# Performance work log

Measured on AMD Instinct MI355X. Metric: run time of the kernel, lower is better.

## Reference

```python
import jax, jax.numpy as jnp
import numpy as np

N = 30000
E = 480000
C_IN, H = 16, 4
NEG_SLOPE = 0.2  # PyG GATv2Conv default negative_slope


def gatv2(x, src, dst, Wl, bl, Wr, br, att, bias, heads, outc, concat, n):
    # PyG GATv2Conv (share_weights=False): e_ij = att . leaky_relu(Wl x_j + Wr x_i)
    xl = (x @ Wl + bl).reshape(n, heads, outc)   # source transform
    xr = (x @ Wr + br).reshape(n, heads, outc)   # target transform
    e = jax.nn.leaky_relu(xl[src] + xr[dst], NEG_SLOPE)        # [E,H,C]
    logits = jnp.einsum('ehc,hc->eh', e, att)                  # [E,H]
    m = jax.lax.stop_gradient(jax.ops.segment_max(logits, dst, num_segments=n))
    ex = jnp.exp(logits - m[dst])
    denom = jax.ops.segment_sum(ex, dst, num_segments=n)
    alpha = ex / denom[dst]                                    # scatter-softmax over in-edges
    out = jax.ops.segment_sum(alpha[:, :, None] * xl[src], dst, num_segments=n)  # [N,H,C]
    out = out.reshape(n, heads * outc) if concat else out.mean(axis=1)
    return out + bias


def setup_inputs() -> dict:
    key = jax.random.key(0)
    ks = jax.random.split(key, 16)
    s = 0.05
    inp = {
        'x': jax.random.uniform(ks[0], (N, C_IN), dtype=jnp.float32),
        'edge_index': jax.random.randint(ks[1], (2, E), 0, N, dtype=jnp.int32),
        'lower_bound': jnp.zeros((C_IN,), jnp.float32),
        'upper_bound': jnp.ones((C_IN,), jnp.float32),
        # Layer 1: GATv2Conv(16 -> 32 per head, heads=4, concat=True) => 128
        'W1l': jax.random.normal(ks[2], (C_IN, H * 32), jnp.float32) * s,
        'b1l': jnp.zeros((H * 32,), jnp.float32),
        'W1r': jax.random.normal(ks[3], (C_IN, H * 32), jnp.float32) * s,
        'b1r': jnp.zeros((H * 32,), jnp.float32),
        'att1': jax.random.normal(ks[4], (H, 32), jnp.float32) * s,
        'bias1': jnp.zeros((H * 32,), jnp.float32),
        # Layer 2: GATv2Conv(128 -> 64 per head, heads=4, concat=False) => 64
        'W2l': jax.random.normal(ks[5], (128, H * 64), jnp.float32) * s,
        'b2l': jnp.zeros((H * 64,), jnp.float32),
        'W2r': jax.random.normal(ks[6], (128, H * 64), jnp.float32) * s,
        'b2r': jnp.zeros((H * 64,), jnp.float32),
        'att2': jax.random.normal(ks[7], (H, 64), jnp.float32) * s,
        'bias2': jnp.zeros((64,), jnp.float32),
        # Final linear head 64 -> 5
        'W3': jax.random.normal(ks[8], (64, 5), jnp.float32) * s,
        'b3': jnp.zeros((5,), jnp.float32),
    }
    return inp


def reference(x, edge_index, lower_bound, upper_bound,
              W1l, b1l, W1r, b1r, att1, bias1,
              W2l, b2l, W2r, b2r, att2, bias2,
              W3, b3):
    n = x.shape[0]
    # min-max normalization
    y = (x - lower_bound) / (upper_bound - lower_bound)
    # add self loops (PyG GATv2Conv default add_self_loops=True)
    loops = jnp.tile(jnp.arange(n, dtype=edge_index.dtype)[None, :], (2, 1))
    ei = jnp.concatenate([edge_index, loops], axis=1)
    src, dst = ei[0], ei[1]
    y = gatv2(y, src, dst, W1l, b1l, W1r, b1r, att1, bias1, H, 32, True, n)
    y = jax.nn.relu(y)
    y = gatv2(y, src, dst, W2l, b2l, W2r, b2r, att2, bias2, H, 64, False, n)
    y = jax.nn.relu(y)
    y = y @ W3 + b3
    return jax.nn.sigmoid(y)
```

## Files before the change

kernel.cpp:

```cpp
#include <hip/hip_runtime.h>

#define H 4
#define D1 128
#define D2 256
#define CIN 16
#define SLOPE 0.2f
#define LOG2E 1.4426950408889634f

typedef short short8v __attribute__((ext_vector_type(8)));
typedef float float4v __attribute__((ext_vector_type(4)));
typedef float float2v __attribute__((ext_vector_type(2)));

__device__ __forceinline__ float bflo(unsigned u) { return __uint_as_float(u << 16); }
__device__ __forceinline__ float bfdirty(unsigned u) { return __uint_as_float(u); }
__device__ __forceinline__ unsigned short f2bf(float f) {
    unsigned int u = __float_as_uint(f);
    u += 0x7FFFu + ((u >> 16) & 1u);
    return (unsigned short)(u >> 16);
}
__device__ __forceinline__ unsigned short f2fp8x2(float a, float b) {
    return (unsigned short)__builtin_amdgcn_cvt_pk_fp8_f32(a, b, 0, false);
}

__global__ void k_hist(const int* __restrict__ ei, int E, int ET,
                       int* __restrict__ deg) {
    int idx = blockIdx.x * blockDim.x + threadIdx.x;
    if (idx >= ET) return;
    int dst = (idx < E) ? ei[E + idx] : idx - E;
    atomicAdd(&deg[dst], 1);
}

__global__ __launch_bounds__(1024) void k_scan_one(
        const int* __restrict__ deg, int* __restrict__ rp,
        int* __restrict__ cur, int n) {
    __shared__ int wsum[16];
    int t = threadIdx.x;
    int lane = t & 63, w = t >> 6;
    int base = t * 32;
    int vals[32];
    const int4* dp = (const int4*)deg;
#pragma unroll
    for (int q = 0; q < 8; ++q) {
        int4 v = dp[(base >> 2) + q];
        vals[4 * q + 0] = v.x; vals[4 * q + 1] = v.y;
        vals[4 * q + 2] = v.z; vals[4 * q + 3] = v.w;
    }
    int loc[32];
    int s = 0;
#pragma unroll
    for (int k = 0; k < 32; ++k) {
        int idx = base + k;
        int v = (idx < n) ? vals[k] : 0;
        loc[k] = s;
        s += v;
    }
    int inc = s;
#pragma unroll
    for (int off = 1; off < 64; off <<= 1) {
        int u = __shfl_up(inc, off, 64);
        if (lane >= off) inc += u;
    }
    int excl = inc - s;
    if (lane == 63) wsum[w] = inc;
    __syncthreads();
    if (w == 0) {
        int v = (lane < 16) ? wsum[lane] : 0;
        int winc = v;
#pragma unroll
        for (int off = 1; off < 16; off <<= 1) {
            int u = __shfl_up(winc, off, 64);
            if (lane >= off) winc += u;
        }
        if (lane < 16) wsum[lane] = winc - v;
    }
    __syncthreads();
    int offw = wsum[w] + excl;
#pragma unroll
    for (int q = 0; q < 8; ++q) {
        int i0 = base + 4 * q;
        if (i0 + 3 < n) {
            *(int4*)(rp + i0) = make_int4(offw + loc[4 * q + 0], offw + loc[4 * q + 1],
                                          offw + loc[4 * q + 2], offw + loc[4 * q + 3]);
            *(int4*)(cur + i0) = make_int4(0, 0, 0, 0);
        } else {
#pragma unroll
            for (int e = 0; e < 4; ++e) {
                int idx = i0 + e;
                if (idx < n) { rp[idx] = offw + loc[4 * q + e]; cur[idx] = 0; }
            }
        }
    }
}

__global__ void k_fill(const int* __restrict__ ei, int E, int ET,
                       const int* __restrict__ rp, int* __restrict__ cur,
                       int* __restrict__ eord) {
    int idx = blockIdx.x * blockDim.x + threadIdx.x;
    if (idx >= ET) return;
    int src, dst;
    if (idx < E) { src = ei[idx]; dst = ei[E + idx]; }
    else         { src = dst = idx - E; }
    int pos = atomicAdd(&cur[dst], 1);
    eord[rp[dst] + pos] = src;
}

__global__ __launch_bounds__(256) void k_prep(
        const float* __restrict__ x, const float* __restrict__ lb,
        const float* __restrict__ ub,
        const float* __restrict__ Wl, const float* __restrict__ bl,
        const float* __restrict__ Wr, const float* __restrict__ br,
        unsigned char* __restrict__ xl8, float* __restrict__ xr,
        const float* __restrict__ W2l, const float* __restrict__ W2r,
        unsigned short* __restrict__ W2t,
        int* __restrict__ deg, int n, int B1) {
    __shared__ float Wls[CIN][D1];
    __shared__ float Wrs[CIN][D1];
    __shared__ float ys[16][CIN];
    int b = blockIdx.x;
    int t = threadIdx.x;
    if (b >= B1) {
        int rb = b - B1;
        if (rb < 256) {
            int idx = rb * 256 + t;
            int k = idx >> 9, c = idx & 511;
            float v = (c < 256) ? W2l[k * 256 + c] : W2r[k * 256 + (c - 256)];
            W2t[(size_t)c * 128 + k] = f2bf(v);
        } else {
            int idx = (rb - 256) * 256 + t;
            if (idx < n) deg[idx] = 0;
        }
        return;
    }
    int i0 = b * 16;
#pragma unroll
    for (int i = 0; i < 8; ++i) {
        int flat = t + 256 * i;
        int k = flat >> 7, c = flat & 127;
        Wls[k][c] = Wl[k * D1 + c];
        Wrs[k][c] = Wr[k * D1 + c];
    }
    {
        int node = t >> 4, k = t & 15;
        int gi = i0 + node;
        float xv = (gi < n) ? x[(size_t)gi * CIN + k] : 0.f;
        ys[node][k] = (xv - lb[k]) / (ub[k] - lb[k]);
    }
    __syncthreads();
    int c = t & 127;
    bool left = t < 128;
    const float (*Ws)[D1] = left ? Wls : Wrs;
    float bias = left ? bl[c] : br[c];
    for (int j = 0; j < 16; ++j) {
        float acc = bias;
#pragma unroll
        for (int k = 0; k < CIN; ++k) acc += ys[j][k] * Ws[k][c];
        int gi = i0 + j;
        float other = __shfl_xor(acc, 1);
        if (gi < n) {
            if (left) {
                if (!(c & 1))
                    *(unsigned short*)(xl8 + (size_t)gi * D1 + c) = f2fp8x2(acc, other);
            } else {
                xr[(size_t)gi * D1 + c] = acc;
            }
        }
    }
}

__global__ __launch_bounds__(256) void k_lin2_mfma(
        const unsigned short* __restrict__ h1b,
        const unsigned short* __restrict__ W2t,
        const float* __restrict__ b2l, const float* __restrict__ b2r,
        unsigned char* __restrict__ xl2,
        unsigned short* __restrict__ xr2,
        int n) {
    __shared__ unsigned short At[128 * 128];
    __shared__ unsigned short Bt[128 * 128];
    int t = threadIdx.x;
    int row0 = blockIdx.x * 128;
    int col0 = blockIdx.y * 128;

    {
        int r = t >> 1, hh = (t & 1) * 64;
        bool ok = (row0 + r) < n;
        const unsigned short* gA = h1b + (size_t)(row0 + r) * 128 + hh;
        const unsigned short* gB = W2t + (size_t)(col0 + r) * 128 + hh;
#pragma unroll
        for (int i = 0; i < 8; ++i) {
            uint4 vA = ok ? *(const uint4*)(gA + i * 8) : make_uint4(0, 0, 0, 0);
            uint4 vB = *(const uint4*)(gB + i * 8);
            int col = hh + i * 8;
            int idx = (r * 128 + col) ^ ((r & 15) << 3);
            *(uint4*)&At[idx] = vA;
            *(uint4*)&Bt[idx] = vB;
        }
    }
    __syncthreads();

    int w = t >> 6, l = t & 63;
    int wr = w >> 1, wc = w & 1;
    float4v acc[4][4];
#pragma unroll
    for (int m = 0; m < 4; ++m)
#pragma unroll
        for (int nn = 0; nn < 4; ++nn) acc[m][nn] = (float4v)0.f;

#pragma unroll
    for (int ks = 0; ks < 4; ++ks) {
        int kb = ks * 32 + ((l >> 4) << 3);
        short8v a[4], b[4];
#pragma unroll
        for (int m = 0; m < 4; ++m) {
            int r = wr * 64 + m * 16 + (l & 15);
            a[m] = *(const short8v*)&At[(r * 128 + kb) ^ ((r & 15) << 3)];
        }
#pragma unroll
        for (int nn = 0; nn < 4; ++nn) {
            int c = wc * 64 + nn * 16 + (l & 15);
            b[nn] = *(const short8v*)&Bt[(c * 128 + kb) ^ ((c & 15) << 3)];
        }
#pragma unroll
        for (int m = 0; m < 4; ++m)
#pragma unroll
            for (int nn = 0; nn < 4; ++nn)
                acc[m][nn] = __builtin_amdgcn_mfma_f32_16x16x32_bf16(
                    a[m], b[nn], acc[m][nn], 0, 0, 0);
    }

    if (col0 < 256) {
        const float* bp = b2l;
        int cb = col0;
#pragma unroll
        for (int nn = 0; nn < 4; ++nn) {
            int colc = cb + wc * 64 + nn * 16 + (l & 15);
            float bv = bp[colc];
#pragma unroll
            for (int m = 0; m < 4; ++m) {
                int rbase = row0 + wr * 64 + m * 16 + ((l >> 4) << 2);
#pragma unroll
                for (int r = 0; r < 4; ++r) {
                    int row = rbase + r;
                    float val = acc[m][nn][r] + bv;
                    float other = __shfl_xor(val, 1);
                    if (!(l & 1) && row < n)
                        *(unsigned short*)(xl2 + (size_t)row * 256 + colc) =
                            f2fp8x2(val, other);
                }
            }
        }
    } else {
        const float* bp = b2r;
        int cb = col0 - 256;
#pragma unroll
        for (int nn = 0; nn < 4; ++nn) {
            int colc = cb + wc * 64 + nn * 16 + (l & 15);
            float bv = bp[colc];
#pragma unroll
            for (int m = 0; m < 4; ++m) {
                int rbase = row0 + wr * 64 + m * 16 + ((l >> 4) << 2);
#pragma unroll
                for (int r = 0; r < 4; ++r) {
                    int row = rbase + r;
                    if (row < n)
                        xr2[(size_t)row * 256 + colc] = f2bf(acc[m][nn][r] + bv);
                }
            }
        }
    }
}

__global__ __launch_bounds__(256) void k_agg1(
        const unsigned char* __restrict__ xl8, const float* __restrict__ xr,
        const float* __restrict__ att, const float* __restrict__ bias,
        const int* __restrict__ rp, const int* __restrict__ deg,
        const int* __restrict__ eord, unsigned short* __restrict__ h1b, int n) {
    int t = threadIdx.x;
    int node = blockIdx.x * 4 + (t >> 6);
    int l = t & 63;
    int nd = (node < n) ? node : n - 1;
    float2 xrv = *(const float2*)(xr + (size_t)nd * D1 + 2 * l);
    float2 av  = *(const float2*)(att + 2 * l);
    av.x *= LOG2E; av.y *= LOG2E;
    int start = __builtin_amdgcn_readfirstlane(rp[nd]);
    int cnt   = (node < n) ? deg[nd] : 0;
    cnt = __builtin_amdgcn_readfirstlane(cnt);
    const unsigned short* xlp = (const unsigned short*)xl8;
    float d = 0.f, a0 = 0.f, a1 = 0.f;
    int cnt4 = cnt & ~3;
    unsigned r0, r1, r2, r3;
    if (cnt4 > 0) {
        int i0 = eord[start + 0], i1 = eord[start + 1];
        int i2 = eord[start + 2], i3 = eord[start + 3];
        r0 = xlp[(size_t)i0 * 64 + l]; r1 = xlp[(size_t)i1 * 64 + l];
        r2 = xlp[(size_t)i2 * 64 + l]; r3 = xlp[(size_t)i3 * 64 + l];
    }
    for (int j = 0; j < cnt4; j += 4) {
        unsigned p0 = r0, p1 = r1, p2 = r2, p3 = r3;
        int jn = j + 4;
        if (jn < cnt4) {
            int i0 = eord[start + jn + 0], i1 = eord[start + jn + 1];
            int i2 = eord[start + jn + 2], i3 = eord[start + jn + 3];
            r0 = xlp[(size_t)i0 * 64 + l]; r1 = xlp[(size_t)i1 * 64 + l];
            r2 = xlp[(size_t)i2 * 64 + l]; r3 = xlp[(size_t)i3 * 64 + l];
        }
        float2v f0 = __builtin_amdgcn_cvt_pk_f32_fp8(p0, false);
        float2v f1 = __builtin_amdgcn_cvt_pk_f32_fp8(p1, false);
        float2v f2 = __builtin_amdgcn_cvt_pk_f32_fp8(p2, false);
        float2v f3 = __builtin_amdgcn_cvt_pk_f32_fp8(p3, false);
        float x00 = f0.x, x01 = f0.y;
        float x10 = f1.x, x11 = f1.y;
        float x20 = f2.x, x21 = f2.y;
        float x30 = f3.x, x31 = f3.y;
        float v, lg0, lg1, lg2, lg3;
        v = x00 + xrv.x; v = fmaxf(v, SLOPE * v); lg0  = av.x * v;
        v = x01 + xrv.y; v = fmaxf(v, SLOPE * v); lg0 += av.y * v;
        v = x10 + xrv.x; v = fmaxf(v, SLOPE * v); lg1  = av.x * v;
        v = x11 + xrv.y; v = fmaxf(v, SLOPE * v); lg1 += av.y * v;
        v = x20 + xrv.x; v = fmaxf(v, SLOPE * v); lg2  = av.x * v;
        v = x21 + xrv.y; v = fmaxf(v, SLOPE * v); lg2 += av.y * v;
        v = x30 + xrv.x; v = fmaxf(v, SLOPE * v); lg3  = av.x * v;
        v = x31 + xrv.y; v = fmaxf(v, SLOPE * v); lg3 += av.y * v;
        lg0 += __shfl_xor(lg0, 8); lg1 += __shfl_xor(lg1, 8);
        lg2 += __shfl_xor(lg2, 8); lg3 += __shfl_xor(lg3, 8);
        lg0 += __shfl_xor(lg0, 4); lg1 += __shfl_xor(lg1, 4);
        lg2 += __shfl_xor(lg2, 4); lg3 += __shfl_xor(lg3, 4);
        lg0 += __shfl_xor(lg0, 2); lg1 += __shfl_xor(lg1, 2);
        lg2 += __shfl_xor(lg2, 2); lg3 += __shfl_xor(lg3, 2);
        lg0 += __shfl_xor(lg0, 1); lg1 += __shfl_xor(lg1, 1);
        lg2 += __shfl_xor(lg2, 1); lg3 += __shfl_xor(lg3, 1);
        float e0 = exp2f(lg0), e1 = exp2f(lg1);
        float e2 = exp2f(lg2), e3 = exp2f(lg3);
        d += (e0 + e1) + (e2 + e3);
        a0 += e0 * x00 + e1 * x10 + e2 * x20 + e3 * x30;
        a1 += e0 * x01 + e1 * x11 + e2 * x21 + e3 * x31;
    }
    for (int j = cnt4; j < cnt; ++j) {
        int s0 = eord[start + j];
        unsigned p0 = xlp[(size_t)s0 * 64 + l];
        float2v f0 = __builtin_amdgcn_cvt_pk_f32_fp8(p0, false);
        float x00 = f0.x, x01 = f0.y;
        float v, lg0;
        v = x00 + xrv.x; v = fmaxf(v, SLOPE * v); lg0  = av.x * v;
        v = x01 + xrv.y; v = fmaxf(v, SLOPE * v); lg0 += av.y * v;
        lg0 += __shfl_xor(lg0, 8);
        lg0 += __shfl_xor(lg0, 4);
        lg0 += __shfl_xor(lg0, 2);
        lg0 += __shfl_xor(lg0, 1);
        float e0 = exp2f(lg0);
        d += e0;
        a0 += e0 * x00;
        a1 += e0 * x01;
    }
    if (node < n) {
        float inv = 1.f / d;
        float o0 = fmaxf(a0 * inv + bias[2 * l + 0], 0.f);
        float o1 = fmaxf(a1 * inv + bias[2 * l + 1], 0.f);
        ((unsigned*)h1b)[(size_t)node * 64 + l] =
            ((unsigned)f2bf(o1) << 16) | f2bf(o0);
    }
}

__global__ __launch_bounds__(256) void k_agg2(
        const unsigned char* __restrict__ xl8, const unsigned short* __restrict__ xr,
        const float* __restrict__ att, const float* __restrict__ b2,
        const float* __restrict__ W3, const float* __restrict__ b3,
        const int* __restrict__ rp, const int* __restrict__ deg,
        const int* __restrict__ eord, float* __restrict__ out, int n) {
    int t = threadIdx.x;
    int node = blockIdx.x * 4 + (t >> 6);
    int l = t & 63;
    int nd = (node < n) ? node : n - 1;
    const uint2* xrp = (const uint2*)xr;
    uint2 xru = xrp[(size_t)nd * 64 + l];
    float4 xrv = make_float4(bflo(xru.x), bfdirty(xru.x), bflo(xru.y), bfdirty(xru.y));
    float4 av  = *(const float4*)(att + 4 * l);
    av.x *= LOG2E; av.y *= LOG2E; av.z *= LOG2E; av.w *= LOG2E;
    int start = __builtin_amdgcn_readfirstlane(rp[nd]);
    int cnt   = (node < n) ? deg[nd] : 0;
    cnt = __builtin_amdgcn_readfirstlane(cnt);
    const unsigned* xlp = (const unsigned*)xl8;
    float d = 0.f, a0 = 0.f, a1 = 0.f, a2 = 0.f, a3 = 0.f;
    int cnt4 = cnt & ~3;
    unsigned r0, r1, r2, r3;
    if (cnt4 > 0) {
        int i0 = eord[start + 0], i1 = eord[start + 1];
        int i2 = eord[start + 2], i3 = eord[start + 3];
        r0 = xlp[(size_t)i0 * 64 + l]; r1 = xlp[(size_t)i1 * 64 + l];
        r2 = xlp[(size_t)i2 * 64 + l]; r3 = xlp[(size_t)i3 * 64 + l];
    }
    for (int j = 0; j < cnt4; j += 4) {
        unsigned p0 = r0, p1 = r1, p2 = r2, p3 = r3;
        int jn = j + 4;
        if (jn < cnt4) {
            int i0 = eord[start + jn + 0], i1 = eord[start + jn + 1];
            int i2 = eord[start + jn + 2], i3 = eord[start + jn + 3];
            r0 = xlp[(size_t)i0 * 64 + l]; r1 = xlp[(size_t)i1 * 64 + l];
            r2 = xlp[(size_t)i2 * 64 + l]; r3 = xlp[(size_t)i3 * 64 + l];
        }
        float2v lo0 = __builtin_amdgcn_cvt_pk_f32_fp8(p0, false);
        float2v hi0 = __builtin_amdgcn_cvt_pk_f32_fp8(p0, true);
        float2v lo1 = __builtin_amdgcn_cvt_pk_f32_fp8(p1, false);
        float2v hi1 = __builtin_amdgcn_cvt_pk_f32_fp8(p1, true);
        float2v lo2 = __builtin_amdgcn_cvt_pk_f32_fp8(p2, false);
        float2v hi2 = __builtin_amdgcn_cvt_pk_f32_fp8(p2, true);
        float2v lo3 = __builtin_amdgcn_cvt_pk_f32_fp8(p3, false);
        float2v hi3 = __builtin_amdgcn_cvt_pk_f32_fp8(p3, true);
        float x00 = lo0.x, x01 = lo0.y, x02 = hi0.x, x03 = hi0.y;
        float x10 = lo1.x, x11 = lo1.y, x12 = hi1.x, x13 = hi1.y;
        float x20 = lo2.x, x21 = lo2.y, x22 = hi2.x, x23 = hi2.y;
        float x30 = lo3.x, x31 = lo3.y, x32 = hi3.x, x33 = hi3.y;
        float v, lg0, lg1, lg2, lg3;
        v = x00 + xrv.x; v = fmaxf(v, SLOPE * v); lg0  = av.x * v;
        v = x01 + xrv.y; v = fmaxf(v, SLOPE * v); lg0 += av.y * v;
        v = x02 + xrv.z; v = fmaxf(v, SLOPE * v); lg0 += av.z * v;
        v = x03 + xrv.w; v = fmaxf(v, SLOPE * v); lg0 += av.w * v;
        v = x10 + xrv.x; v = fmaxf(v, SLOPE * v); lg1  = av.x * v;
        v = x11 + xrv.y; v = fmaxf(v, SLOPE * v); lg1 += av.y * v;
        v = x12 + xrv.z; v = fmaxf(v, SLOPE * v); lg1 += av.z * v;
        v = x13 + xrv.w; v = fmaxf(v, SLOPE * v); lg1 += av.w * v;
        v = x20 + xrv.x; v = fmaxf(v, SLOPE * v); lg2  = av.x * v;
        v = x21 + xrv.y; v = fmaxf(v, SLOPE * v); lg2 += av.y * v;
        v = x22 + xrv.z; v = fmaxf(v, SLOPE * v); lg2 += av.z * v;
        v = x23 + xrv.w; v = fmaxf(v, SLOPE * v); lg2 += av.w * v;
        v = x30 + xrv.x; v = fmaxf(v, SLOPE * v); lg3  = av.x * v;
        v = x31 + xrv.y; v = fmaxf(v, SLOPE * v); lg3 += av.y * v;
        v = x32 + xrv.z; v = fmaxf(v, SLOPE * v); lg3 += av.z * v;
        v = x33 + xrv.w; v = fmaxf(v, SLOPE * v); lg3 += av.w * v;
        lg0 += __shfl_xor(lg0, 8); lg1 += __shfl_xor(lg1, 8);
        lg2 += __shfl_xor(lg2, 8); lg3 += __shfl_xor(lg3, 8);
        lg0 += __shfl_xor(lg0, 4); lg1 += __shfl_xor(lg1, 4);
        lg2 += __shfl_xor(lg2, 4); lg3 += __shfl_xor(lg3, 4);
        lg0 += __shfl_xor(lg0, 2); lg1 += __shfl_xor(lg1, 2);
        lg2 += __shfl_xor(lg2, 2); lg3 += __shfl_xor(lg3, 2);
        lg0 += __shfl_xor(lg0, 1); lg1 += __shfl_xor(lg1, 1);
        lg2 += __shfl_xor(lg2, 1); lg3 += __shfl_xor(lg3, 1);
        float e0 = exp2f(lg0), e1 = exp2f(lg1);
        float e2 = exp2f(lg2), e3 = exp2f(lg3);
        d += (e0 + e1) + (e2 + e3);
        a0 += e0 * x00 + e1 * x10 + e2 * x20 + e3 * x30;
        a1 += e0 * x01 + e1 * x11 + e2 * x21 + e3 * x31;
        a2 += e0 * x02 + e1 * x12 + e2 * x22 + e3 * x32;
        a3 += e0 * x03 + e1 * x13 + e2 * x23 + e3 * x33;
    }
    for (int j = cnt4; j < cnt; ++j) {
        int s0 = eord[start + j];
        unsigned p0 = xlp[(size_t)s0 * 64 + l];
        float2v lo0 = __builtin_amdgcn_cvt_pk_f32_fp8(p0, false);
        float2v hi0 = __builtin_amdgcn_cvt_pk_f32_fp8(p0, true);
        float x00 = lo0.x, x01 = lo0.y, x02 = hi0.x, x03 = hi0.y;
        float v, lg0;
        v = x00 + xrv.x; v = fmaxf(v, SLOPE * v); lg0  = av.x * v;
        v = x01 + xrv.y; v = fmaxf(v, SLOPE * v); lg0 += av.y * v;
        v = x02 + xrv.z; v = fmaxf(v, SLOPE * v); lg0 += av.z * v;
        v = x03 + xrv.w; v = fmaxf(v, SLOPE * v); lg0 += av.w * v;
        lg0 += __shfl_xor(lg0, 8);
        lg0 += __shfl_xor(lg0, 4);
        lg0 += __shfl_xor(lg0, 2);
        lg0 += __shfl_xor(lg0, 1);
        float e0 = exp2f(lg0);
        d += e0;
        a0 += e0 * x00; a1 += e0 * x01; a2 += e0 * x02; a3 += e0 * x03;
    }
    float inv = 1.f / d;
    float v0 = a0 * inv, v1 = a1 * inv, v2 = a2 * inv, v3 = a3 * inv;
    v0 += __shfl_xor(v0, 16); v1 += __shfl_xor(v1, 16);
    v2 += __shfl_xor(v2, 16); v3 += __shfl_xor(v3, 16);
    v0 += __shfl_xor(v0, 32); v1 += __shfl_xor(v1, 32);
    v2 += __shfl_xor(v2, 32); v3 += __shfl_xor(v3, 32);
    int c0 = 4 * (l & 15);
    v0 = fmaxf(0.25f * v0 + b2[c0 + 0], 0.f);
    v1 = fmaxf(0.25f * v1 + b2[c0 + 1], 0.f);
    v2 = fmaxf(0.25f * v2 + b2[c0 + 2], 0.f);
    v3 = fmaxf(0.25f * v3 + b2[c0 + 3], 0.f);
    float p0, p1, p2, p3, p4;
    {
        const float* w0 = W3 + (c0 + 0) * 5;
        const float* w1 = W3 + (c0 + 1) * 5;
        const float* w2 = W3 + (c0 + 2) * 5;
        const float* w3 = W3 + (c0 + 3) * 5;
        p0 = v0 * w0[0] + v1 * w1[0] + v2 * w2[0] + v3 * w3[0];
        p1 = v0 * w0[1] + v1 * w1[1] + v2 * w2[1] + v3 * w3[1];
        p2 = v0 * w0[2] + v1 * w1[2] + v2 * w2[2] + v3 * w3[2];
        p3 = v0 * w0[3] + v1 * w1[3] + v2 * w2[3] + v3 * w3[3];
        p4 = v0 * w0[4] + v1 * w1[4] + v2 * w2[4] + v3 * w3[4];
    }
#pragma unroll
    for (int off = 1; off < 16; off <<= 1) {
        p0 += __shfl_xor(p0, off); p1 += __shfl_xor(p1, off);
        p2 += __shfl_xor(p2, off); p3 += __shfl_xor(p3, off);
        p4 += __shfl_xor(p4, off);
    }
    if (l == 0 && node < n) {
        float* o = out + (size_t)node * 5;
        o[0] = 1.f / (1.f + __expf(-(p0 + b3[0])));
        o[1] = 1.f / (1.f + __expf(-(p1 + b3[1])));
        o[2] = 1.f / (1.f + __expf(-(p2 + b3[2])));
        o[3] = 1.f / (1.f + __expf(-(p3 + b3[3])));
        o[4] = 1.f / (1.f + __expf(-(p4 + b3[4])));
    }
}

extern "C" void kernel_launch(void* const* d_in, const int* in_sizes, int n_in,
                              void* d_out, int out_size, void* d_ws, size_t ws_size,
                              hipStream_t stream) {
    const float* x     = (const float*)d_in[0];
    const int*   ei    = (const int*)d_in[1];
    const float* lb    = (const float*)d_in[2];
    const float* ub    = (const float*)d_in[3];
    const float* W1l   = (const float*)d_in[4];
    const float* b1l   = (const float*)d_in[5];
    const float* W1r   = (const float*)d_in[6];
    const float* b1r   = (const float*)d_in[7];
    const float* att1  = (const float*)d_in[8];
    const float* bias1 = (const float*)d_in[9];
    const float* W2l   = (const float*)d_in[10];
    const float* b2l   = (const float*)d_in[11];
    const float* W2r   = (const float*)d_in[12];
    const float* b2r   = (const float*)d_in[13];
    const float* att2  = (const float*)d_in[14];
    const float* bias2 = (const float*)d_in[15];
    const float* W3    = (const float*)d_in[16];
    const float* b3    = (const float*)d_in[17];

    int n  = in_sizes[0] / CIN;
    int E  = in_sizes[1] / 2;
    int ET = E + n;

    char* ws = (char*)d_ws;
    size_t off = 0;
    auto alloc = [&](size_t nbytes) {
        void* p = ws + off;
        off += (nbytes + 255) & ~(size_t)255;
        return p;
    };
    unsigned char*  xl1 = (unsigned char*)alloc((size_t)n * D1);
    float*          xr1 = (float*)alloc((size_t)n * D1 * 4);
    unsigned short* h1b = (unsigned short*)alloc((size_t)n * D1 * 2);
    unsigned char*  xl2 = (unsigned char*)alloc((size_t)n * D2);
    unsigned short* xr2 = (unsigned short*)alloc((size_t)n * D2 * 2);
    unsigned short* W2t = (unsigned short*)alloc((size_t)512 * 128 * 2);
    int* deg  = (int*)alloc((size_t)n * 4 + 8192);
    int* cur  = (int*)alloc((size_t)n * 4);
    int* rp   = (int*)alloc((size_t)n * 4);
    int* eord = (int*)alloc((size_t)ET * 4);

    int B1 = (n + 15) / 16;
    int BZ = (n + 255) / 256;
    k_prep<<<B1 + 256 + BZ, 256, 0, stream>>>(
        x, lb, ub, W1l, b1l, W1r, b1r, xl1, xr1, W2l, W2r, W2t, deg, n, B1);

    k_hist<<<(ET + 255) / 256, 256, 0, stream>>>(ei, E, ET, deg);
    k_scan_one<<<1, 1024, 0, stream>>>(deg, rp, cur, n);
    k_fill<<<(ET + 255) / 256, 256, 0, stream>>>(ei, E, ET, rp, cur, eord);

    k_agg1<<<(n + 3) / 4, 256, 0, stream>>>(xl1, xr1, att1, bias1, rp, deg,
                                            eord, h1b, n);

    dim3 g2((n + 127) / 128, 4);
    k_lin2_mfma<<<g2, 256, 0, stream>>>(h1b, W2t, b2l, b2r, xl2, xr2, n);
    k_agg2<<<(n + 3) / 4, 256, 0, stream>>>(xl2, xr2, att2, bias2, W3, b3,
                                            rp, deg, eord, (float*)d_out, n);
}
```

Baseline: 181.7 us.

## Deepen gather prefetch pipeline in aggregation kernels with masked tail

Restructures the per-node edge loops in both aggregation kernels. Three groups of four source-row gathers are now kept in flight, and edge indices are prefetched one group ahead, replacing the previous single group of lookahead. The separate scalar remainder loop is gone. Index reads are clamped to the last valid edge and out-of-range contributions are zeroed, so the loop can run in fixed chunks of 12. The aim is to hide gather latency in these memory-latency-bound loops, at the cost of more live registers and up to 8 wasted masked edge evaluations per node.

```diff
diff --git a/kernel.cpp b/kernel.cpp
--- a/kernel.cpp
+++ b/kernel.cpp
@@ -284,73 +284,81 @@
     int start = __builtin_amdgcn_readfirstlane(rp[nd]);
     int cnt   = (node < n) ? deg[nd] : 0;
     cnt = __builtin_amdgcn_readfirstlane(cnt);
+    int ecl = (cnt > 0) ? cnt - 1 : 0;
     const unsigned short* xlp = (const unsigned short*)xl8;
     float d = 0.f, a0 = 0.f, a1 = 0.f;
-    int cnt4 = cnt & ~3;
-    unsigned r0, r1, r2, r3;
-    if (cnt4 > 0) {
-        int i0 = eord[start + 0], i1 = eord[start + 1];
-        int i2 = eord[start + 2], i3 = eord[start + 3];
-        r0 = xlp[(size_t)i0 * 64 + l]; r1 = xlp[(size_t)i1 * 64 + l];
-        r2 = xlp[(size_t)i2 * 64 + l]; r3 = xlp[(size_t)i3 * 64 + l];
-    }
-    for (int j = 0; j < cnt4; j += 4) {
-        unsigned p0 = r0, p1 = r1, p2 = r2, p3 = r3;
-        int jn = j + 4;
-        if (jn < cnt4) {
-            int i0 = eord[start + jn + 0], i1 = eord[start + jn + 1];
-            int i2 = eord[start + jn + 2], i3 = eord[start + jn + 3];
-            r0 = xlp[(size_t)i0 * 64 + l]; r1 = xlp[(size_t)i1 * 64 + l];
-            r2 = xlp[(size_t)i2 * 64 + l]; r3 = xlp[(size_t)i3 * 64 + l];
-        }
-        float2v f0 = __builtin_amdgcn_cvt_pk_f32_fp8(p0, false);
-        float2v f1 = __builtin_amdgcn_cvt_pk_f32_fp8(p1, false);
-        float2v f2 = __builtin_amdgcn_cvt_pk_f32_fp8(p2, false);
-        float2v f3 = __builtin_amdgcn_cvt_pk_f32_fp8(p3, false);
-        float x00 = f0.x, x01 = f0.y;
-        float x10 = f1.x, x11 = f1.y;
-        float x20 = f2.x, x21 = f2.y;
-        float x30 = f3.x, x31 = f3.y;
-        float v, lg0, lg1, lg2, lg3;
-        v = x00 + xrv.x; v = fmaxf(v, SLOPE * v); lg0  = av.x * v;
-        v = x01 + xrv.y; v = fmaxf(v, SLOPE * v); lg0 += av.y * v;
-        v = x10 + xrv.x; v = fmaxf(v, SLOPE * v); lg1  = av.x * v;
-        v = x11 + xrv.y; v = fmaxf(v, SLOPE * v); lg1 += av.y * v;
-        v = x20 + xrv.x; v = fmaxf(v, SLOPE * v); lg2  = av.x * v;
-        v = x21 + xrv.y; v = fmaxf(v, SLOPE * v); lg2 += av.y * v;
-        v = x30 + xrv.x; v = fmaxf(v, SLOPE * v); lg3  = av.x * v;
-        v = x31 + xrv.y; v = fmaxf(v, SLOPE * v); lg3 += av.y * v;
-        lg0 += __shfl_xor(lg0, 8); lg1 += __shfl_xor(lg1, 8);
-        lg2 += __shfl_xor(lg2, 8); lg3 += __shfl_xor(lg3, 8);
-        lg0 += __shfl_xor(lg0, 4); lg1 += __shfl_xor(lg1, 4);
-        lg2 += __shfl_xor(lg2, 4); lg3 += __shfl_xor(lg3, 4);
-        lg0 += __shfl_xor(lg0, 2); lg1 += __shfl_xor(lg1, 2);
-        lg2 += __shfl_xor(lg2, 2); lg3 += __shfl_xor(lg3, 2);
-        lg0 += __shfl_xor(lg0, 1); lg1 += __shfl_xor(lg1, 1);
-        lg2 += __shfl_xor(lg2, 1); lg3 += __shfl_xor(lg3, 1);
-        float e0 = exp2f(lg0), e1 = exp2f(lg1);
-        float e2 = exp2f(lg2), e3 = exp2f(lg3);
-        d += (e0 + e1) + (e2 + e3);
-        a0 += e0 * x00 + e1 * x10 + e2 * x20 + e3 * x30;
-        a1 += e0 * x01 + e1 * x11 + e2 * x21 + e3 * x31;
-    }
-    for (int j = cnt4; j < cnt; ++j) {
-        int s0 = eord[start + j];
-        unsigned p0 = xlp[(size_t)s0 * 64 + l];
-        float2v f0 = __builtin_amdgcn_cvt_pk_f32_fp8(p0, false);
-        float x00 = f0.x, x01 = f0.y;
-        float v, lg0;
-        v = x00 + xrv.x; v = fmaxf(v, SLOPE * v); lg0  = av.x * v;
-        v = x01 + xrv.y; v = fmaxf(v, SLOPE * v); lg0 += av.y * v;
-        lg0 += __shfl_xor(lg0, 8);
-        lg0 += __shfl_xor(lg0, 4);
-        lg0 += __shfl_xor(lg0, 2);
-        lg0 += __shfl_xor(lg0, 1);
-        float e0 = exp2f(lg0);
-        d += e0;
-        a0 += e0 * x00;
-        a1 += e0 * x01;
-    }
+    int cntR = (cnt + 3) & ~3;
+
+    unsigned gA[4], gB[4], gC[4];
+    int4 iD;
+    if (cntR > 0) {
+        int4 iA, iB, iC;
+        iA.x = eord[start + min(0, ecl)];  iA.y = eord[start + min(1, ecl)];
+        iA.z = eord[start + min(2, ecl)];  iA.w = eord[start + min(3, ecl)];
+        iB.x = eord[start + min(4, ecl)];  iB.y = eord[start + min(5, ecl)];
+        iB.z = eord[start + min(6, ecl)];  iB.w = eord[start + min(7, ecl)];
+        iC.x = eord[start + min(8, ecl)];  iC.y = eord[start + min(9, ecl)];
+        iC.z = eord[start + min(10, ecl)]; iC.w = eord[start + min(11, ecl)];
+        gA[0] = xlp[(size_t)iA.x * 64 + l]; gA[1] = xlp[(size_t)iA.y * 64 + l];
+        gA[2] = xlp[(size_t)iA.z * 64 + l]; gA[3] = xlp[(size_t)iA.w * 64 + l];
+        gB[0] = xlp[(size_t)iB.x * 64 + l]; gB[1] = xlp[(size_t)iB.y * 64 + l];
+        gB[2] = xlp[(size_t)iB.z * 64 + l]; gB[3] = xlp[(size_t)iB.w * 64 + l];
+        gC[0] = xlp[(size_t)iC.x * 64 + l]; gC[1] = xlp[(size_t)iC.y * 64 + l];
+        gC[2] = xlp[(size_t)iC.z * 64 + l]; gC[3] = xlp[(size_t)iC.w * 64 + l];
+        iD.x = eord[start + min(12, ecl)]; iD.y = eord[start + min(13, ecl)];
+        iD.z = eord[start + min(14, ecl)]; iD.w = eord[start + min(15, ecl)];
+    }
+
+#define A1_BODY(G, JB)                                                         \
+    {                                                                          \
+        unsigned p0 = G[0], p1 = G[1], p2 = G[2], p3 = G[3];                   \
+        G[0] = xlp[(size_t)iD.x * 64 + l]; G[1] = xlp[(size_t)iD.y * 64 + l];  \
+        G[2] = xlp[(size_t)iD.z * 64 + l]; G[3] = xlp[(size_t)iD.w * 64 + l];  \
+        iD.x = eord[start + min((JB) + 16, ecl)];                              \
+        iD.y = eord[start + min((JB) + 17, ecl)];                              \
+        iD.z = eord[start + min((JB) + 18, ecl)];                              \
+        iD.w = eord[start + min((JB) + 19, ecl)];                              \
+        float2v f0 = __builtin_amdgcn_cvt_pk_f32_fp8(p0, false);               \
+        float2v f1 = __builtin_amdgcn_cvt_pk_f32_fp8(p1, false);               \
+        float2v f2 = __builtin_amdgcn_cvt_pk_f32_fp8(p2, false);               \
+        float2v f3 = __builtin_amdgcn_cvt_pk_f32_fp8(p3, false);               \
+        float v, lg0, lg1, lg2, lg3;                                           \
+        v = f0.x + xrv.x; v = fmaxf(v, SLOPE * v); lg0  = av.x * v;            \
+        v = f0.y + xrv.y; v = fmaxf(v, SLOPE * v); lg0 += av.y * v;            \
+        v = f1.x + xrv.x; v = fmaxf(v, SLOPE * v); lg1  = av.x * v;            \
+        v = f1.y + xrv.y; v = fmaxf(v, SLOPE * v); lg1 += av.y * v;            \
+        v = f2.x + xrv.x; v = fmaxf(v, SLOPE * v); lg2  = av.x * v;            \
+        v = f2.y + xrv.y; v = fmaxf(v, SLOPE * v); lg2 += av.y * v;            \
+        v = f3.x + xrv.x; v = fmaxf(v, SLOPE * v); lg3  = av.x * v;            \
+        v = f3.y + xrv.y; v = fmaxf(v, SLOPE * v); lg3 += av.y * v;            \
+        lg0 += __shfl_xor(lg0, 8); lg1 += __shfl_xor(lg1, 8);                  \
+        lg2 += __shfl_xor(lg2, 8); lg3 += __shfl_xor(lg3, 8);                  \
+        lg0 += __shfl_xor(lg0, 4); lg1 += __shfl_xor(lg1, 4);                  \
+        lg2 += __shfl_xor(lg2, 4); lg3 += __shfl_xor(lg3, 4);                  \
+        lg0 += __shfl_xor(lg0, 2); lg1 += __shfl_xor(lg1, 2);                  \
+        lg2 += __shfl_xor(lg2, 2); lg3 += __shfl_xor(lg3, 2);                  \
+        lg0 += __shfl_xor(lg0, 1); lg1 += __shfl_xor(lg1, 1);                  \
+        lg2 += __shfl_xor(lg2, 1); lg3 += __shfl_xor(lg3, 1);                  \
+        float e0 = exp2f(lg0), e1 = exp2f(lg1);                                \
+        float e2 = exp2f(lg2), e3 = exp2f(lg3);                                \
+        if ((JB) + 3 > ecl) {                                                  \
+            if ((JB) > ecl)     e0 = 0.f;                                      \
+            if ((JB) + 1 > ecl) e1 = 0.f;                                      \
+            if ((JB) + 2 > ecl) e2 = 0.f;                                      \
+            if ((JB) + 3 > ecl) e3 = 0.f;                                      \
+        }                                                                      \
+        d += (e0 + e1) + (e2 + e3);                                            \
+        a0 += e0 * f0.x + e1 * f1.x + e2 * f2.x + e3 * f3.x;                   \
+        a1 += e0 * f0.y + e1 * f1.y + e2 * f2.y + e3 * f3.y;                   \
+    }
+
+    for (int jb = 0; jb < cntR; jb += 12) {
+        A1_BODY(gA, jb);
+        A1_BODY(gB, jb + 4);
+        A1_BODY(gC, jb + 8);
+    }
+#undef A1_BODY
+
     if (node < n) {
         float inv = 1.f / d;
         float o0 = fmaxf(a0 * inv + bias[2 * l + 0], 0.f);
@@ -378,89 +386,95 @@
     int start = __builtin_amdgcn_readfirstlane(rp[nd]);
     int cnt   = (node < n) ? deg[nd] : 0;
     cnt = __builtin_amdgcn_readfirstlane(cnt);
+    int ecl = (cnt > 0) ? cnt - 1 : 0;
     const unsigned* xlp = (const unsigned*)xl8;
     float d = 0.f, a0 = 0.f, a1 = 0.f, a2 = 0.f, a3 = 0.f;
-    int cnt4 = cnt & ~3;
-    unsigned r0, r1, r2, r3;
-    if (cnt4 > 0) {
-        int i0 = eord[start + 0], i1 = eord[start + 1];
-        int i2 = eord[start + 2], i3 = eord[start + 3];
-        r0 = xlp[(size_t)i0 * 64 + l]; r1 = xlp[(size_t)i1 * 64 + l];
-        r2 = xlp[(size_t)i2 * 64 + l]; r3 = xlp[(size_t)i3 * 64 + l];
-    }
-    for (int j = 0; j < cnt4; j += 4) {
-        unsigned p0 = r0, p1 = r1, p2 = r2, p3 = r3;
-        int jn = j + 4;
-        if (jn < cnt4) {
-            int i0 = eord[start + jn + 0], i1 = eord[start + jn + 1];
-            int i2 = eord[start + jn + 2], i3 = eord[start + jn + 3];
-            r0 = xlp[(size_t)i0 * 64 + l]; r1 = xlp[(size_t)i1 * 64 + l];
-            r2 = xlp[(size_t)i2 * 64 + l]; r3 = xlp[(size_t)i3 * 64 + l];
-        }
-        float2v lo0 = __builtin_amdgcn_cvt_pk_f32_fp8(p0, false);
-        float2v hi0 = __builtin_amdgcn_cvt_pk_f32_fp8(p0, true);
-        float2v lo1 = __builtin_amdgcn_cvt_pk_f32_fp8(p1, false);
-        float2v hi1 = __builtin_amdgcn_cvt_pk_f32_fp8(p1, true);
-        float2v lo2 = __builtin_amdgcn_cvt_pk_f32_fp8(p2, false);
-        float2v hi2 = __builtin_amdgcn_cvt_pk_f32_fp8(p2, true);
-        float2v lo3 = __builtin_amdgcn_cvt_pk_f32_fp8(p3, false);
-        float2v hi3 = __builtin_amdgcn_cvt_pk_f32_fp8(p3, true);
-        float x00 = lo0.x, x01 = lo0.y, x02 = hi0.x, x03 = hi0.y;
-        float x10 = lo1.x, x11 = lo1.y, x12 = hi1.x, x13 = hi1.y;
-        float x20 = lo2.x, x21 = lo2.y, x22 = hi2.x, x23 = hi2.y;
-        float x30 = lo3.x, x31 = lo3.y, x32 = hi3.x, x33 = hi3.y;
-        float v, lg0, lg1, lg2, lg3;
-        v = x00 + xrv.x; v = fmaxf(v, SLOPE * v); lg0  = av.x * v;
-        v = x01 + xrv.y; v = fmaxf(v, SLOPE * v); lg0 += av.y * v;
-        v = x02 + xrv.z; v = fmaxf(v, SLOPE * v); lg0 += av.z * v;
-        v = x03 + xrv.w; v = fmaxf(v, SLOPE * v); lg0 += av.w * v;
-        v = x10 + xrv.x; v = fmaxf(v, SLOPE * v); lg1  = av.x * v;
-        v = x11 + xrv.y; v = fmaxf(v, SLOPE * v); lg1 += av.y * v;
-        v = x12 + xrv.z; v = fmaxf(v, SLOPE * v); lg1 += av.z * v;
-        v = x13 + xrv.w; v = fmaxf(v, SLOPE * v); lg1 += av.w * v;
-        v = x20 + xrv.x; v = fmaxf(v, SLOPE * v); lg2  = av.x * v;
-        v = x21 + xrv.y; v = fmaxf(v, SLOPE * v); lg2 += av.y * v;
-        v = x22 + xrv.z; v = fmaxf(v, SLOPE * v); lg2 += av.z * v;
-        v = x23 + xrv.w; v = fmaxf(v, SLOPE * v); lg2 += av.w * v;
-        v = x30 + xrv.x; v = fmaxf(v, SLOPE * v); lg3  = av.x * v;
-        v = x31 + xrv.y; v = fmaxf(v, SLOPE * v); lg3 += av.y * v;
-        v = x32 + xrv.z; v = fmaxf(v, SLOPE * v); lg3 += av.z * v;
-        v = x33 + xrv.w; v = fmaxf(v, SLOPE * v); lg3 += av.w * v;
-        lg0 += __shfl_xor(lg0, 8); lg1 += __shfl_xor(lg1, 8);
-        lg2 += __shfl_xor(lg2, 8); lg3 += __shfl_xor(lg3, 8);
-        lg0 += __shfl_xor(lg0, 4); lg1 += __shfl_xor(lg1, 4);
-        lg2 += __shfl_xor(lg2, 4); lg3 += __shfl_xor(lg3, 4);
-        lg0 += __shfl_xor(lg0, 2); lg1 += __shfl_xor(lg1, 2);
-        lg2 += __shfl_xor(lg2, 2); lg3 += __shfl_xor(lg3, 2);
-        lg0 += __shfl_xor(lg0, 1); lg1 += __shfl_xor(lg1, 1);
-        lg2 += __shfl_xor(lg2, 1); lg3 += __shfl_xor(lg3, 1);
-        float e0 = exp2f(lg0), e1 = exp2f(lg1);
-        float e2 = exp2f(lg2), e3 = exp2f(lg3);
-        d += (e0 + e1) + (e2 + e3);
-        a0 += e0 * x00 + e1 * x10 + e2 * x20 + e3 * x30;
-        a1 += e0 * x01 + e1 * x11 + e2 * x21 + e3 * x31;
-        a2 += e0 * x02 + e1 * x12 + e2 * x22 + e3 * x32;
-        a3 += e0 * x03 + e1 * x13 + e2 * x23 + e3 * x33;
-    }
-    for (int j = cnt4; j < cnt; ++j) {
-        int s0 = eord[start + j];
-        unsigned p0 = xlp[(size_t)s0 * 64 + l];
-        float2v lo0 = __builtin_amdgcn_cvt_pk_f32_fp8(p0, false);
-        float2v hi0 = __builtin_amdgcn_cvt_pk_f32_fp8(p0, true);
-        float x00 = lo0.x, x01 = lo0.y, x02 = hi0.x, x03 = hi0.y;
-        float v, lg0;
-        v = x00 + xrv.x; v = fmaxf(v, SLOPE * v); lg0  = av.x * v;
-        v = x01 + xrv.y; v = fmaxf(v, SLOPE * v); lg0 += av.y * v;
-        v = x02 + xrv.z; v = fmaxf(v, SLOPE * v); lg0 += av.z * v;
-        v = x03 + xrv.w; v = fmaxf(v, SLOPE * v); lg0 += av.w * v;
-        lg0 += __shfl_xor(lg0, 8);
-        lg0 += __shfl_xor(lg0, 4);
-        lg0 += __shfl_xor(lg0, 2);
-        lg0 += __shfl_xor(lg0, 1);
-        float e0 = exp2f(lg0);
-        d += e0;
-        a0 += e0 * x00; a1 += e0 * x01; a2 += e0 * x02; a3 += e0 * x03;
-    }
+    int cntR = (cnt + 3) & ~3;
+
+    unsigned gA[4], gB[4], gC[4];
+    int4 iD;
+    if (cntR > 0) {
+        int4 iA, iB, iC;
+        iA.x = eord[start + min(0, ecl)];  iA.y = eord[start + min(1, ecl)];
+        iA.z = eord[start + min(2, ecl)];  iA.w = eord[start + min(3, ecl)];
+        iB.x = eord[start + min(4, ecl)];  iB.y = eord[start + min(5, ecl)];
+        iB.z = eord[start + min(6, ecl)];  iB.w = eord[start + min(7, ecl)];
+        iC.x = eord[start + min(8, ecl)];  iC.y = eord[start + min(9, ecl)];
+        iC.z = eord[start + min(10, ecl)]; iC.w = eord[start + min(11, ecl)];
+        gA[0] = xlp[(size_t)iA.x * 64 + l]; gA[1] = xlp[(size_t)iA.y * 64 + l];
+        gA[2] = xlp[(size_t)iA.z * 64 + l]; gA[3] = xlp[(size_t)iA.w * 64 + l];
+        gB[0] = xlp[(size_t)iB.x * 64 + l]; gB[1] = xlp[(size_t)iB.y * 64 + l];
+        gB[2] = xlp[(size_t)iB.z * 64 + l]; gB[3] = xlp[(size_t)iB.w * 64 + l];
+        gC[0] = xlp[(size_t)iC.x * 64 + l]; gC[1] = xlp[(size_t)iC.y * 64 + l];
+        gC[2] = xlp[(size_t)iC.z * 64 + l]; gC[3] = xlp[(size_t)iC.w * 64 + l];
+        iD.x = eord[start + min(12, ecl)]; iD.y = eord[start + min(13, ecl)];
+        iD.z = eord[start + min(14, ecl)]; iD.w = eord[start + min(15, ecl)];
+    }
+
+#define A2_BODY(G, JB)                                                         \
+    {                                                                          \
+        unsigned p0 = G[0], p1 = G[1], p2 = G[2], p3 = G[3];                   \
+        G[0] = xlp[(size_t)iD.x * 64 + l]; G[1] = xlp[(size_t)iD.y * 64 + l];  \
+        G[2] = xlp[(size_t)iD.z * 64 + l]; G[3] = xlp[(size_t)iD.w * 64 + l];  \
+        iD.x = eord[start + min((JB) + 16, ecl)];                              \
+        iD.y = eord[start + min((JB) + 17, ecl)];                              \
+        iD.z = eord[start + min((JB) + 18, ecl)];                              \
+        iD.w = eord[start + min((JB) + 19, ecl)];                              \
+        float2v lo0 = __builtin_amdgcn_cvt_pk_f32_fp8(p0, false);              \
+        float2v hi0 = __builtin_amdgcn_cvt_pk_f32_fp8(p0, true);               \
+        float2v lo1 = __builtin_amdgcn_cvt_pk_f32_fp8(p1, false);              \
+        float2v hi1 = __builtin_amdgcn_cvt_pk_f32_fp8(p1, true);               \
+        float2v lo2 = __builtin_amdgcn_cvt_pk_f32_fp8(p2, false);              \
+        float2v hi2 = __builtin_amdgcn_cvt_pk_f32_fp8(p2, true);               \
+        float2v lo3 = __builtin_amdgcn_cvt_pk_f32_fp8(p3, false);              \
+        float2v hi3 = __builtin_amdgcn_cvt_pk_f32_fp8(p3, true);               \
+        float v, lg0, lg1, lg2, lg3;                                           \
+        v = lo0.x + xrv.x; v = fmaxf(v, SLOPE * v); lg0  = av.x * v;           \
+        v = lo0.y + xrv.y; v = fmaxf(v, SLOPE * v); lg0 += av.y * v;           \
+        v = hi0.x + xrv.z; v = fmaxf(v, SLOPE * v); lg0 += av.z * v;           \
+        v = hi0.y + xrv.w; v = fmaxf(v, SLOPE * v); lg0 += av.w * v;           \
+        v = lo1.x + xrv.x; v = fmaxf(v, SLOPE * v); lg1  = av.x * v;           \
+        v = lo1.y + xrv.y; v = fmaxf(v, SLOPE * v); lg1 += av.y * v;           \
+        v = hi1.x + xrv.z; v = fmaxf(v, SLOPE * v); lg1 += av.z * v;           \
+        v = hi1.y + xrv.w; v = fmaxf(v, SLOPE * v); lg1 += av.w * v;           \
+        v = lo2.x + xrv.x; v = fmaxf(v, SLOPE * v); lg2  = av.x * v;           \
+        v = lo2.y + xrv.y; v = fmaxf(v, SLOPE * v); lg2 += av.y * v;           \
+        v = hi2.x + xrv.z; v = fmaxf(v, SLOPE * v); lg2 += av.z * v;           \
+        v = hi2.y + xrv.w; v = fmaxf(v, SLOPE * v); lg2 += av.w * v;           \
+        v = lo3.x + xrv.x; v = fmaxf(v, SLOPE * v); lg3  = av.x * v;           \
+        v = lo3.y + xrv.y; v = fmaxf(v, SLOPE * v); lg3 += av.y * v;           \
+        v = hi3.x + xrv.z; v = fmaxf(v, SLOPE * v); lg3 += av.z * v;           \
+        v = hi3.y + xrv.w; v = fmaxf(v, SLOPE * v); lg3 += av.w * v;           \
+        lg0 += __shfl_xor(lg0, 8); lg1 += __shfl_xor(lg1, 8);                  \
+        lg2 += __shfl_xor(lg2, 8); lg3 += __shfl_xor(lg3, 8);                  \
+        lg0 += __shfl_xor(lg0, 4); lg1 += __shfl_xor(lg1, 4);                  \
+        lg2 += __shfl_xor(lg2, 4); lg3 += __shfl_xor(lg3, 4);                  \
+        lg0 += __shfl_xor(lg0, 2); lg1 += __shfl_xor(lg1, 2);                  \
+        lg2 += __shfl_xor(lg2, 2); lg3 += __shfl_xor(lg3, 2);                  \
+        lg0 += __shfl_xor(lg0, 1); lg1 += __shfl_xor(lg1, 1);                  \
+        lg2 += __shfl_xor(lg2, 1); lg3 += __shfl_xor(lg3, 1);                  \
+        float e0 = exp2f(lg0), e1 = exp2f(lg1);                                \
+        float e2 = exp2f(lg2), e3 = exp2f(lg3);                                \
+        if ((JB) + 3 > ecl) {                                                  \
+            if ((JB) > ecl)     e0 = 0.f;                                      \
+            if ((JB) + 1 > ecl) e1 = 0.f;                                      \
+            if ((JB) + 2 > ecl) e2 = 0.f;                                      \
+            if ((JB) + 3 > ecl) e3 = 0.f;                                      \
+        }                                                                      \
+        d += (e0 + e1) + (e2 + e3);                                            \
+        a0 += e0 * lo0.x + e1 * lo1.x + e2 * lo2.x + e3 * lo3.x;               \
+        a1 += e0 * lo0.y + e1 * lo1.y + e2 * lo2.y + e3 * lo3.y;               \
+        a2 += e0 * hi0.x + e1 * hi1.x + e2 * hi2.x + e3 * hi3.x;               \
+        a3 += e0 * hi0.y + e1 * hi1.y + e2 * hi2.y + e3 * hi3.y;               \
+    }
+
+    for (int jb = 0; jb < cntR; jb += 12) {
+        A2_BODY(gA, jb);
+        A2_BODY(gB, jb + 4);
+        A2_BODY(gC, jb + 8);
+    }
+#undef A2_BODY
+
     float inv = 1.f / d;
     float v0 = a0 * inv, v1 = a1 * inv, v2 = a2 * inv, v3 = a3 * inv;
     v0 += __shfl_xor(v0, 16); v1 += __shfl_xor(v1, 16);
```

Result: slower. 204.1 us (+12.4%).
